# Kernel tuning notes

Hardware: AMD Instinct MI355X
Metric: run time of the kernel (lower is better)

Reference implementation:

```python
import jax, jax.numpy as jnp
import numpy as np
from jax import lax

EPS = 1e-8

def _cosine_cost(x, y):
    # 1 - cosine_similarity over feature dim: [B,N,M]
    xn = x / jnp.clip(jnp.linalg.norm(x, axis=-1, keepdims=True), EPS)
    yn = y / jnp.clip(jnp.linalg.norm(y, axis=-1, keepdims=True), EPS)
    return 1.0 - jnp.einsum('bnd,bmd->bnm', xn, yn)

def _dtw_table(cost):
    # cost: [B,N,M] -> cumulative cost tc: [B,N,M]
    # tc[i,j] = cost[i,j] + min(tc[i-1,j-1], tc[i-1,j], tc[i,j-1])
    B, N, M = cost.shape
    row0 = jnp.cumsum(cost[:, 0, :], axis=1)  # [B,M]

    def col_step(left, inp):
        c, pdiag, pup = inp  # each [B]
        v = c + jnp.minimum(jnp.minimum(pdiag, pup), left)
        return v, v

    def row_step(prev, cost_row):
        # prev, cost_row: [B,M]
        first = prev[:, 0] + cost_row[:, 0]  # [B]
        xs = (cost_row[:, 1:].T, prev[:, :-1].T, prev[:, 1:].T)  # [M-1,B]
        _, rest = lax.scan(col_step, first, xs)  # [M-1,B]
        row = jnp.concatenate([first[:, None], rest.T], axis=1)  # [B,M]
        return row, row

    _, rows = lax.scan(row_step, row0, jnp.swapaxes(cost[:, 1:, :], 0, 1))
    tc = jnp.concatenate([row0[:, None, :], jnp.swapaxes(rows, 0, 1)], axis=1)
    return tc

def _backtrack(tc):
    # tc: [N,M] -> 0/1 path matrix [N,M]; tie-break diag > up > left,
    # matching the torch equality-chain order.
    N, M = tc.shape
    path0 = jnp.zeros((N, M), tc.dtype).at[N - 1, M - 1].set(1.0)

    def cond(s):
        i, j, _ = s
        return jnp.logical_and(i > 0, j > 0)

    def body(s):
        i, j, p = s
        a = tc[i - 1, j - 1]
        b = tc[i - 1, j]
        c = tc[i, j - 1]
        diag = jnp.logical_and(a <= b, a <= c)
        up = jnp.logical_and(jnp.logical_not(diag), b <= c)
        ni = jnp.where(jnp.logical_or(diag, up), i - 1, i)
        nj = jnp.where(jnp.logical_or(diag, jnp.logical_not(up)), j - 1, j)
        p = p.at[ni, nj].set(1.0)
        return ni, nj, p

    _, _, p = lax.while_loop(cond, body, (jnp.int32(N - 1), jnp.int32(M - 1), path0))
    return p.at[0, 0].set(1.0)

def setup_inputs() -> dict:
    key = jax.random.key(0)
    kx, ky = jax.random.split(key)
    B, N, M, D = 64, 512, 512, 256
    x = jax.random.normal(kx, (B, N, D), dtype=jnp.float32)
    y = jax.random.normal(ky, (B, M, D), dtype=jnp.float32)
    return {"x": x, "y": y}

def reference(x, y):
    cost = _cosine_cost(x, y)                 # [B,N,M]
    tc = _dtw_table(cost)                     # [B,N,M]
    path = jax.vmap(_backtrack)(tc)           # [B,N,M]
    pos = jax.nn.logsumexp(jnp.sum(cost * path, axis=1), axis=1)  # [B]
    neg = jax.nn.logsumexp(jnp.sum(cost, axis=1), axis=1)         # [B]
    return pos - neg
```

## Files before the change

### kernel.cpp

```cpp
#include <hip/hip_runtime.h>
#include <hip/hip_bf16.h>
#include <stdint.h>

typedef __attribute__((ext_vector_type(8))) short short8v;
typedef __attribute__((ext_vector_type(4))) float float4v;
typedef __attribute__((ext_vector_type(4))) unsigned short ushort4v;
typedef __attribute__((ext_vector_type(4))) unsigned int uint4v;

#define FINF __builtin_huge_valf()
#define BB 64
#define NN 512
#define DD 256
#define TT_SKEW 640


static __device__ __forceinline__ unsigned short f2bf(float f) {
  union { float f; uint32_t u; } a; a.f = f;
  uint32_t r = a.u + 0x7fffu + ((a.u >> 16) & 1u);
  return (unsigned short)(r >> 16);
}
static __device__ __forceinline__ float bf2f(uint16_t v) {
  return __uint_as_float(((uint32_t)v) << 16);
}

__global__ __launch_bounds__(64) void pad_zero_kernel(uint16_t* __restrict__ skew)
{
  const int tau = blockIdx.x, b = blockIdx.y, g = threadIdx.x;
  const int r = tau - 2 * g;
  if (r < 0 || r > 511) {
    uint16_t* p = skew + ((size_t)b * TT_SKEW + tau) * NN + g * 8;
    *(uint4v*)p = (uint4v){0u, 0u, 0u, 0u};
  }
}

__global__ __launch_bounds__(256) void norm_cast_kernel(
    const float* __restrict__ x, const float* __restrict__ y,
    uint16_t* __restrict__ xnb, uint16_t* __restrict__ ynb)
{
  const int wave = threadIdx.x >> 6, lane = threadIdx.x & 63;
  const int row = blockIdx.x * 4 + wave;
  const float* src; uint16_t* dst;
  if (row < BB * NN) { src = x + (size_t)row * DD;            dst = xnb + (size_t)row * DD; }
  else               { src = y + (size_t)(row - BB*NN) * DD;  dst = ynb + (size_t)(row - BB*NN) * DD; }
  const float4v v = *(const float4v*)(src + lane * 4);
  float s = v[0]*v[0] + v[1]*v[1] + v[2]*v[2] + v[3]*v[3];
  #pragma unroll
  for (int d = 1; d < 64; d <<= 1) s += __shfl_xor(s, d, 64);
  const float inv = 1.0f / fmaxf(sqrtf(s), 1e-8f);
  ushort4v o;
  o[0] = f2bf(v[0] * inv); o[1] = f2bf(v[1] * inv);
  o[2] = f2bf(v[2] * inv); o[3] = f2bf(v[3] * inv);
  *(ushort4v*)(dst + lane * 4) = o;
}

__global__ __launch_bounds__(256) void gemm_cost_kernel(
    const uint16_t* __restrict__ xnb, const uint16_t* __restrict__ ynb,
    uint16_t* __restrict__ skew)
{
  __shared__ uint16_t As[128 * 32];
  __shared__ uint16_t Bs[128 * 32];
  const int bid = blockIdx.x;
  const int b = bid >> 4, tm = (bid >> 2) & 3, tn = bid & 3;
  const int tid = threadIdx.x, wave = tid >> 6, lane = tid & 63;
  const int wr = wave >> 1, wc = wave & 1;

  const char* Ab = (const char*)(xnb + (size_t)b * NN * DD + (size_t)tm * 128 * DD);
  const char* Bb = (const char*)(ynb + (size_t)b * NN * DD + (size_t)tn * 128 * DD);

  float4v acc[4][4];
  #pragma unroll
  for (int i = 0; i < 4; i++)
    #pragma unroll
    for (int j = 0; j < 4; j++) acc[i][j] = (float4v){0.f, 0.f, 0.f, 0.f};

  const int seg0 = wave * 2;
  const int o0 = seg0 * 1024 + lane * 16;
  const int o1 = o0 + 1024;
  const int r0 = o0 >> 6, c0 = o0 & 63;
  const int r1 = o1 >> 6, c1 = o1 & 63;

  for (int kk = 0; kk < 8; kk++) {
    const int kb = kk * 64;
    __builtin_amdgcn_global_load_lds(
        (const __attribute__((address_space(1))) uint32_t*)(Ab + (size_t)r0 * 512 + kb + c0),
        (__attribute__((address_space(3))) uint32_t*)((char*)As + seg0 * 1024), 16, 0, 0);
    __builtin_amdgcn_global_load_lds(
        (const __attribute__((address_space(1))) uint32_t*)(Ab + (size_t)r1 * 512 + kb + c1),
        (__attribute__((address_space(3))) uint32_t*)((char*)As + (seg0 + 1) * 1024), 16, 0, 0);
    __builtin_amdgcn_global_load_lds(
        (const __attribute__((address_space(1))) uint32_t*)(Bb + (size_t)r0 * 512 + kb + c0),
        (__attribute__((address_space(3))) uint32_t*)((char*)Bs + seg0 * 1024), 16, 0, 0);
    __builtin_amdgcn_global_load_lds(
        (const __attribute__((address_space(1))) uint32_t*)(Bb + (size_t)r1 * 512 + kb + c1),
        (__attribute__((address_space(3))) uint32_t*)((char*)Bs + (seg0 + 1) * 1024), 16, 0, 0);
    __syncthreads();

    short8v af[4], bfr[4];
    #pragma unroll
    for (int mi = 0; mi < 4; mi++) {
      const int rr = wr * 64 + mi * 16 + (lane & 15);
      af[mi] = *(const short8v*)((const char*)As + rr * 64 + (lane >> 4) * 16);
    }
    #pragma unroll
    for (int nj = 0; nj < 4; nj++) {
      const int rr = wc * 64 + nj * 16 + (lane & 15);
      bfr[nj] = *(const short8v*)((const char*)Bs + rr * 64 + (lane >> 4) * 16);
    }
    #pragma unroll
    for (int mi = 0; mi < 4; mi++)
      #pragma unroll
      for (int nj = 0; nj < 4; nj++)
        acc[mi][nj] = __builtin_amdgcn_mfma_f32_16x16x32_bf16(af[mi], bfr[nj], acc[mi][nj], 0, 0, 0);
    __syncthreads();
  }

  uint16_t* Cb = skew + (size_t)b * TT_SKEW * NN;
  #pragma unroll
  for (int mi = 0; mi < 4; mi++)
    #pragma unroll
    for (int nj = 0; nj < 4; nj++) {
      const int cc = tn * 128 + wc * 64 + nj * 16 + (lane & 15);
      const int lg = cc >> 3;
      #pragma unroll
      for (int v = 0; v < 4; v++) {
        const int rr = tm * 128 + wr * 64 + mi * 16 + (lane >> 4) * 4 + v;
        Cb[(size_t)(rr + 2 * lg) * NN + cc] = f2bf(1.0f - acc[mi][nj][v]);
      }
    }
}

__global__ __launch_bounds__(256) void neg_lse_kernel(
    const uint16_t* __restrict__ skew, float* __restrict__ negbuf)
{
  __shared__ float sm[8];
  const int b = blockIdx.x, tid = threadIdx.x;
  const int wave = tid >> 6, lane = tid & 63;
  const uint32_t* p = (const uint32_t*)(skew + (size_t)b * TT_SKEW * NN) + tid;
  float s0 = 0.f, s1 = 0.f;
  #pragma unroll 8
  for (int t = 0; t < TT_SKEW; ++t) {
    const uint32_t w = p[t * 256];
    s0 += __uint_as_float(w << 16);
    s1 += __uint_as_float(w & 0xFFFF0000u);
  }
  float m = fmaxf(s0, s1);
  #pragma unroll
  for (int d = 1; d < 64; d <<= 1) m = fmaxf(m, __shfl_xor(m, d, 64));
  if (lane == 0) sm[wave] = m;
  __syncthreads();
  m = fmaxf(fmaxf(sm[0], sm[1]), fmaxf(sm[2], sm[3]));
  float e = expf(s0 - m) + expf(s1 - m);
  #pragma unroll
  for (int d = 1; d < 64; d <<= 1) e += __shfl_xor(e, d, 64);
  if (lane == 0) sm[4 + wave] = e;
  __syncthreads();
  if (tid == 0) negbuf[b] = m + logf(sm[4] + sm[5] + sm[6] + sm[7]);
}

__global__ __launch_bounds__(64, 1) void dtw_fwd_kernel(
    const uint16_t* __restrict__ skew, uint32_t* __restrict__ decg)
{
  extern __shared__ char lds_raw[];
  const int l = threadIdx.x;
  const int b = blockIdx.x;
  const uint16_t* csk = skew + (size_t)b * TT_SKEW * NN;
  const uint64_t base = (uint64_t)(uintptr_t)csk;
  const bool is0 = (l == 0);
  const uint32_t voff_base = 16u * (uint32_t)l;

  uint4v ringA[8], ringB[8];
  #pragma unroll
  for (int i = 0; i < 8; ++i) {
    const uint32_t voA = voff_base + ((uint32_t)(2 * i) << 10);
    const uint32_t voB = voA + 1024u;
    asm volatile("global_load_dwordx4 %0, %1, %2" : "=v"(ringA[i]) : "v"(voA), "s"(base));
    asm volatile("global_load_dwordx4 %0, %1, %2" : "=v"(ringB[i]) : "v"(voB), "s"(base));
  }

  float tp[8];
  #pragma unroll
  for (int c = 0; c < 8; ++c) tp[c] = FINF;
  float cl0 = FINF, cl1 = FINF, carry = FINF;
  const uint32_t dump_addr = 65536u + (((uint32_t)l) << 2);

  for (int t0 = 0; t0 < 320; t0 += 8) {
    #pragma unroll
    for (int u = 0; u < 8; ++u) {
      const int t = t0 + u;
      float shA = __shfl_up(cl0, 1, 64);
      float shB = __shfl_up(cl1, 1, 64);
      if (is0) { shA = (t == 0) ? 0.0f : FINF; shB = FINF; }
      const float sh_p0 = carry;
      carry = shB;

      asm volatile("s_waitcnt vmcnt(14)" : "+v"(ringA[u]), "+v"(ringB[u]));
      const uint4v A = ringA[u];
      const uint4v Bv = ringB[u];

      const uint32_t rlane = (uint32_t)(t - l);
      const bool valid = rlane < 256u;

      float ca[8], cbv[8], S0[8], S1[8];
      #pragma unroll
      for (int k = 0; k < 4; ++k) {
        ca[2*k]   = __uint_as_float(A[k] << 16);
        ca[2*k+1] = __uint_as_float(A[k] & 0xFFFF0000u);
        cbv[2*k]   = __uint_as_float(Bv[k] << 16);
        cbv[2*k+1] = __uint_as_float(Bv[k] & 0xFFFF0000u);
      }
      S0[0] = ca[0]; S1[0] = cbv[0];
      #pragma unroll
      for (int c = 1; c < 8; ++c) { S0[c] = S0[c-1] + ca[c]; S1[c] = S1[c-1] + cbv[c]; }

      float dcp0[8], mu0[8], w0[8], PW0[8], tn0[8];
      dcp0[0] = sh_p0;
      #pragma unroll
      for (int c = 1; c < 8; ++c) dcp0[c] = tp[c-1];
      #pragma unroll
      for (int c = 0; c < 8; ++c) mu0[c] = fminf(dcp0[c], tp[c]);
      w0[0] = mu0[0];
      #pragma unroll
      for (int c = 1; c < 8; ++c) w0[c] = mu0[c] - S0[c-1];
      PW0[0] = w0[0];
      #pragma unroll
      for (int c = 1; c < 8; ++c) PW0[c] = fminf(PW0[c-1], w0[c]);
      #pragma unroll
      for (int c = 0; c < 8; ++c) tn0[c] = fminf(PW0[c], shA) + S0[c];

      float dcp1[8], mu1[8], w1[8], PW1[8], tn1[8];
      dcp1[0] = shA;
      #pragma unroll
      for (int c = 1; c < 8; ++c) dcp1[c] = tn0[c-1];
      #pragma unroll
      for (int c = 0; c < 8; ++c) mu1[c] = fminf(dcp1[c], tn0[c]);
      w1[0] = mu1[0];
      #pragma unroll
      for (int c = 1; c < 8; ++c) w1[c] = mu1[c] - S1[c-1];
      PW1[0] = w1[0];
      #pragma unroll
      for (int c = 1; c < 8; ++c) PW1[c] = fminf(PW1[c-1], w1[c]);
      #pragma unroll
      for (int c = 0; c < 8; ++c) tn1[c] = fminf(PW1[c], shB) + S1[c];

      uint32_t word = 0;
      {
        float lc0[8], lc1[8];
        lc0[0] = shA; lc1[0] = shB;
        #pragma unroll
        for (int c = 1; c < 8; ++c) { lc0[c] = tn0[c-1]; lc1[c] = tn1[c-1]; }
        #pragma unroll
        for (int c = 0; c < 8; ++c) {
          const uint32_t e0 = (tp[c] < dcp0[c]) ? 1u : 0u;
          const uint32_t d0 = (lc0[c] < mu0[c]) ? 2u : e0;
          const uint32_t e1 = (tn0[c] < dcp1[c]) ? 1u : 0u;
          const uint32_t d1 = (lc1[c] < mu1[c]) ? 2u : e1;
          word |= (d0 << (2 * c)) | (d1 << (16 + 2 * c));
        }
      }
      const uint32_t waddr = valid ? ((rlane << 8) | (((uint32_t)l) << 2)) : dump_addr;
      *(uint32_t*)(lds_raw + waddr) = word;

      #pragma unroll
      for (int c = 0; c < 8; ++c) tp[c] = valid ? tn1[c] : tp[c];
      cl0 = valid ? tn0[7] : cl0;
      cl1 = tp[7];

      {
        int rr = 2 * (t + 8); if (rr > 638) rr = 638;
        const uint32_t voA = voff_base + ((uint32_t)rr << 10);
        const uint32_t voB = voA + 1024u;
        asm volatile("global_load_dwordx4 %0, %1, %2" : "=v"(ringA[u]) : "v"(voA), "s"(base));
        asm volatile("global_load_dwordx4 %0, %1, %2" : "=v"(ringB[u]) : "v"(voB), "s"(base));
      }
    }
  }
  asm volatile("s_waitcnt vmcnt(0)" ::: "memory");

  uint32_t* dg = decg + (size_t)b * 16384;
  #pragma unroll 4
  for (int i = 0; i < 64; ++i)
    *(uint4v*)(dg + i * 256 + l * 4) = *(const uint4v*)(lds_raw + i * 1024 + l * 16);
}

__global__ __launch_bounds__(64, 1) void dtw_bt_kernel(
    const uint16_t* __restrict__ skew, const uint32_t* __restrict__ decg,
    const float* __restrict__ negbuf, float* __restrict__ out)
{
  extern __shared__ char lds_raw[];
  uint16_t* rlo    = (uint16_t*)(lds_raw + 65536);
  uint16_t* rhi    = (uint16_t*)(lds_raw + 66560);
  float*    colpos = (float*)  (lds_raw + 67584);
  const uint32_t* dec32 = (const uint32_t*)lds_raw;

  const int l = threadIdx.x;
  const int b = blockIdx.x;
  const uint16_t* csk = skew + (size_t)b * TT_SKEW * NN;
  const uint32_t* dg = decg + (size_t)b * 16384;

  #pragma unroll 4
  for (int i = 0; i < 64; ++i)
    *(uint4v*)(lds_raw + i * 1024 + l * 16) = *(const uint4v*)(dg + i * 256 + l * 4);
  for (int r = l; r < NN; r += 64) { rlo[r] = 1; rhi[r] = 0; colpos[r] = 0.0f; }
  __syncthreads();

  if (l == 0) {
    int i = NN - 1, j = NN - 1, hicur = NN - 1;
    int cidx = -1; uint32_t cw = 0;
    while (i > 0 && j > 0) {
      const int widx = (i >> 1) * 64 + (j >> 3);
      if (widx != cidx) { cw = dec32[widx]; cidx = widx; }
      const uint32_t dd = (cw >> (((i & 1) << 4) + ((j & 7) << 1))) & 3u;
      if (dd == 2u) { j--; }
      else {
        rlo[i] = (uint16_t)j; rhi[i] = (uint16_t)hicur;
        i--;
        if (dd == 0u) j--;
        hicur = j;
      }
    }
    rlo[i] = (uint16_t)j; rhi[i] = (uint16_t)hicur;
  }
  __syncthreads();
  for (int r = l; r < NN; r += 64) {
    const int lo = rlo[r], hi = rhi[r];
    for (int j = lo; j <= hi; j++) {
      const float cv = bf2f(csk[(size_t)(r + 2 * (j >> 3)) * NN + j]);
      atomicAdd(&colpos[j], cv);
    }
  }
  if (l == 0 && rlo[0] != 0) atomicAdd(&colpos[0], bf2f(csk[0]));
  __syncthreads();

  float mv[8];
  float mx2 = -FINF;
  #pragma unroll
  for (int k = 0; k < 8; k++) { mv[k] = colpos[l + 64 * k]; mx2 = fmaxf(mx2, mv[k]); }
  #pragma unroll
  for (int d = 1; d < 64; d <<= 1) mx2 = fmaxf(mx2, __shfl_xor(mx2, d, 64));
  float se2 = 0.f;
  #pragma unroll
  for (int k = 0; k < 8; k++) se2 += expf(mv[k] - mx2);
  #pragma unroll
  for (int d = 1; d < 64; d <<= 1) se2 += __shfl_xor(se2, d, 64);
  const float pos = mx2 + logf(se2);

  if (l == 0) out[b] = pos - negbuf[b];
}

extern "C" void kernel_launch(void* const* d_in, const int* in_sizes, int n_in,
                              void* d_out, int out_size, void* d_ws, size_t ws_size,
                              hipStream_t stream)
{
  (void)in_sizes; (void)n_in; (void)out_size; (void)ws_size;
  const float* x = (const float*)d_in[0];
  const float* y = (const float*)d_in[1];
  float* out = (float*)d_out;
  char* ws = (char*)d_ws;
  uint16_t* xnb  = (uint16_t*)ws;
  uint16_t* ynb  = (uint16_t*)(ws + (size_t)16777216);
  uint16_t* skew = (uint16_t*)(ws + (size_t)33554432);
  float*  negbuf = (float*)  (ws + (size_t)75497472);
  uint32_t* decg = (uint32_t*)(ws + (size_t)75501568);

  (void)hipFuncSetAttribute((const void*)dtw_fwd_kernel,
                            hipFuncAttributeMaxDynamicSharedMemorySize, 65792);
  (void)hipFuncSetAttribute((const void*)dtw_bt_kernel,
                            hipFuncAttributeMaxDynamicSharedMemorySize, 69632);

  pad_zero_kernel<<<dim3(TT_SKEW, BB), 64, 0, stream>>>(skew);
  norm_cast_kernel<<<16384, 256, 0, stream>>>(x, y, xnb, ynb);
  gemm_cost_kernel<<<1024, 256, 0, stream>>>(xnb, ynb, skew);
  neg_lse_kernel<<<64, 256, 0, stream>>>(skew, negbuf);
  dtw_fwd_kernel<<<64, 64, 65792, stream>>>(skew, decg);
  dtw_bt_kernel<<<64, 64, 69632, stream>>>(skew, decg, negbuf, out);
}
```

Baseline: 297.9 us.

## Drop pad kernel, fuse neg LSE into backtrack, pack DTW waves per block

Removes the zero-padding kernel and the separate neg-LSE kernel. The neg-LSE column sums now run inside a 256-thread backtrack kernel that also reads only the 512 valid skew rows per lane group. The forward DTW kernel now runs eight batches per 512-thread block, writing decision words straight to global memory instead of staging them in LDS, and uses a 4-deep load ring instead of 8. Backtracking reads decision words in 4x8 chunks to cut repeated LDS loads. The risks are less latency hiding in the serial DTW loop from the shallower prefetch, scattered global stores, and correctness of the skipped padding, which now depends on the loads never consuming pad cells.

```diff
diff --git a/kernel.cpp b/kernel.cpp
--- a/kernel.cpp
+++ b/kernel.cpp
@@ -21,16 +21,6 @@
 }
 static __device__ __forceinline__ float bf2f(uint16_t v) {
   return __uint_as_float(((uint32_t)v) << 16);
-}
-
-__global__ __launch_bounds__(64) void pad_zero_kernel(uint16_t* __restrict__ skew)
-{
-  const int tau = blockIdx.x, b = blockIdx.y, g = threadIdx.x;
-  const int r = tau - 2 * g;
-  if (r < 0 || r > 511) {
-    uint16_t* p = skew + ((size_t)b * TT_SKEW + tau) * NN + g * 8;
-    *(uint4v*)p = (uint4v){0u, 0u, 0u, 0u};
-  }
 }
 
 __global__ __launch_bounds__(256) void norm_cast_kernel(
@@ -129,222 +119,227 @@
     }
 }
 
-__global__ __launch_bounds__(256) void neg_lse_kernel(
-    const uint16_t* __restrict__ skew, float* __restrict__ negbuf)
-{
-  __shared__ float sm[8];
-  const int b = blockIdx.x, tid = threadIdx.x;
-  const int wave = tid >> 6, lane = tid & 63;
-  const uint32_t* p = (const uint32_t*)(skew + (size_t)b * TT_SKEW * NN) + tid;
-  float s0 = 0.f, s1 = 0.f;
-  #pragma unroll 8
-  for (int t = 0; t < TT_SKEW; ++t) {
-    const uint32_t w = p[t * 256];
-    s0 += __uint_as_float(w << 16);
-    s1 += __uint_as_float(w & 0xFFFF0000u);
-  }
-  float m = fmaxf(s0, s1);
-  #pragma unroll
-  for (int d = 1; d < 64; d <<= 1) m = fmaxf(m, __shfl_xor(m, d, 64));
-  if (lane == 0) sm[wave] = m;
-  __syncthreads();
-  m = fmaxf(fmaxf(sm[0], sm[1]), fmaxf(sm[2], sm[3]));
-  float e = expf(s0 - m) + expf(s1 - m);
-  #pragma unroll
-  for (int d = 1; d < 64; d <<= 1) e += __shfl_xor(e, d, 64);
-  if (lane == 0) sm[4 + wave] = e;
-  __syncthreads();
-  if (tid == 0) negbuf[b] = m + logf(sm[4] + sm[5] + sm[6] + sm[7]);
-}
-
-__global__ __launch_bounds__(64, 1) void dtw_fwd_kernel(
-    const uint16_t* __restrict__ skew, uint32_t* __restrict__ decg)
-{
-  extern __shared__ char lds_raw[];
-  const int l = threadIdx.x;
-  const int b = blockIdx.x;
-  const uint16_t* csk = skew + (size_t)b * TT_SKEW * NN;
-  const uint64_t base = (uint64_t)(uintptr_t)csk;
+__global__ __launch_bounds__(512, 2) void dtw_fwd_kernel(
+    const uint16_t* __restrict__ skew, uint32_t* __restrict__ decg,
+    uint32_t* __restrict__ dumpg)
+{
+  const int tid = threadIdx.x;
+  const int wv = tid >> 6, l = tid & 63;
+  const int batch = blockIdx.x * 8 + wv;
+  const uint16_t* csk = skew + (size_t)batch * TT_SKEW * NN;
+  uint32_t* const dw = decg + (size_t)batch * 16384;
+  const uintptr_t dmp_addr = (uintptr_t)(dumpg + l);
+  const uint64_t base64 = (uint64_t)(uintptr_t)csk + 16u * (uint32_t)l;
   const bool is0 = (l == 0);
-  const uint32_t voff_base = 16u * (uint32_t)l;
-
-  uint4v ringA[8], ringB[8];
-  #pragma unroll
-  for (int i = 0; i < 8; ++i) {
-    const uint32_t voA = voff_base + ((uint32_t)(2 * i) << 10);
-    const uint32_t voB = voA + 1024u;
-    asm volatile("global_load_dwordx4 %0, %1, %2" : "=v"(ringA[i]) : "v"(voA), "s"(base));
-    asm volatile("global_load_dwordx4 %0, %1, %2" : "=v"(ringB[i]) : "v"(voB), "s"(base));
+
+  uint4v rA[4], rB[4];
+  #pragma unroll
+  for (int i = 0; i < 4; ++i) {
+    const uint64_t aA = base64 + ((uint64_t)(2 * i) << 10);
+    asm volatile("global_load_dwordx4 %0, %1, off" : "=v"(rA[i]) : "v"(aA));
+    asm volatile("global_load_dwordx4 %0, %1, off" : "=v"(rB[i]) : "v"(aA + 1024u));
   }
 
   float tp[8];
   #pragma unroll
   for (int c = 0; c < 8; ++c) tp[c] = FINF;
   float cl0 = FINF, cl1 = FINF, carry = FINF;
-  const uint32_t dump_addr = 65536u + (((uint32_t)l) << 2);
-
-  for (int t0 = 0; t0 < 320; t0 += 8) {
-    #pragma unroll
-    for (int u = 0; u < 8; ++u) {
+
+  auto STEP = [&](int t, const uint4v A, const uint4v Bv) {
+    float shA = __shfl_up(cl0, 1, 64);
+    float shB = __shfl_up(cl1, 1, 64);
+    if (is0) { shA = (t == 0) ? 0.0f : FINF; shB = FINF; }
+    const float sh_p0 = carry;
+    carry = shB;
+    const float shA1 = is0 ? FINF : shA;
+
+    const uint32_t rlane = (uint32_t)(t - l);
+    const bool valid = rlane < 256u;
+
+    float ca[8], cb[8], S0[8], S1[8];
+    #pragma unroll
+    for (int k = 0; k < 4; ++k) {
+      ca[2*k]   = __uint_as_float(A[k] << 16);
+      ca[2*k+1] = __uint_as_float(A[k] & 0xFFFF0000u);
+      cb[2*k]   = __uint_as_float(Bv[k] << 16);
+      cb[2*k+1] = __uint_as_float(Bv[k] & 0xFFFF0000u);
+    }
+    S0[0] = ca[0]; S1[0] = cb[0];
+    #pragma unroll
+    for (int c = 1; c < 8; ++c) { S0[c] = S0[c-1] + ca[c]; S1[c] = S1[c-1] + cb[c]; }
+
+    float dcp0[8], mu0[8], w0[8], PW0[8], tn0[8];
+    dcp0[0] = sh_p0;
+    #pragma unroll
+    for (int c = 1; c < 8; ++c) dcp0[c] = tp[c-1];
+    #pragma unroll
+    for (int c = 0; c < 8; ++c) mu0[c] = fminf(dcp0[c], tp[c]);
+    w0[0] = mu0[0];
+    #pragma unroll
+    for (int c = 1; c < 8; ++c) w0[c] = mu0[c] - S0[c-1];
+    PW0[0] = w0[0];
+    #pragma unroll
+    for (int c = 1; c < 8; ++c) PW0[c] = fminf(PW0[c-1], w0[c]);
+    #pragma unroll
+    for (int c = 0; c < 8; ++c) tn0[c] = fminf(PW0[c], shA) + S0[c];
+
+    float dcp1[8], mu1[8], w1[8], PW1[8], tn1[8];
+    dcp1[0] = shA1;
+    #pragma unroll
+    for (int c = 1; c < 8; ++c) dcp1[c] = tn0[c-1];
+    #pragma unroll
+    for (int c = 0; c < 8; ++c) mu1[c] = fminf(dcp1[c], tn0[c]);
+    w1[0] = mu1[0];
+    #pragma unroll
+    for (int c = 1; c < 8; ++c) w1[c] = mu1[c] - S1[c-1];
+    PW1[0] = w1[0];
+    #pragma unroll
+    for (int c = 1; c < 8; ++c) PW1[c] = fminf(PW1[c-1], w1[c]);
+    #pragma unroll
+    for (int c = 0; c < 8; ++c) tn1[c] = fminf(PW1[c], shB) + S1[c];
+
+    uint32_t word = 0;
+    {
+      float lc0[8], lc1[8];
+      lc0[0] = shA; lc1[0] = shB;
+      #pragma unroll
+      for (int c = 1; c < 8; ++c) { lc0[c] = tn0[c-1]; lc1[c] = tn1[c-1]; }
+      #pragma unroll
+      for (int c = 0; c < 8; ++c) {
+        const uint32_t e0 = (tp[c] < dcp0[c]) ? 1u : 0u;
+        const uint32_t d0 = (lc0[c] < mu0[c]) ? 2u : e0;
+        const uint32_t e1 = (tn0[c] < dcp1[c]) ? 1u : 0u;
+        const uint32_t d1 = (lc1[c] < mu1[c]) ? 2u : e1;
+        word |= (d0 << (2 * c)) | (d1 << (16 + 2 * c));
+      }
+    }
+    const uintptr_t dsta = valid ? (uintptr_t)(dw + (rlane << 6) + l) : dmp_addr;
+    *(uint32_t*)dsta = word;
+
+    #pragma unroll
+    for (int c = 0; c < 8; ++c) tp[c] = valid ? tn1[c] : tp[c];
+    cl0 = valid ? tn0[7] : cl0;
+    cl1 = tp[7];
+  };
+
+  auto RELOAD = [&](int u, int t) {
+    int rr = 2 * (t + 4); if (rr > 638) rr = 638;
+    const uint64_t aA = base64 + ((uint64_t)rr << 10);
+    asm volatile("global_load_dwordx4 %0, %1, off" : "=v"(rA[u]) : "v"(aA));
+    asm volatile("global_load_dwordx4 %0, %1, off" : "=v"(rB[u]) : "v"(aA + 1024u));
+  };
+
+  asm volatile("s_waitcnt vmcnt(6)" : "+v"(rA[0]), "+v"(rB[0]) : : "memory");
+  STEP(0, rA[0], rB[0]); RELOAD(0, 0);
+  asm volatile("s_waitcnt vmcnt(7)" : "+v"(rA[1]), "+v"(rB[1]) : : "memory");
+  STEP(1, rA[1], rB[1]); RELOAD(1, 1);
+  asm volatile("s_waitcnt vmcnt(8)" : "+v"(rA[2]), "+v"(rB[2]) : : "memory");
+  STEP(2, rA[2], rB[2]); RELOAD(2, 2);
+  asm volatile("s_waitcnt vmcnt(9)" : "+v"(rA[3]), "+v"(rB[3]) : : "memory");
+  STEP(3, rA[3], rB[3]); RELOAD(3, 3);
+
+  for (int t0 = 4; t0 < 320; t0 += 4) {
+    #pragma unroll
+    for (int u = 0; u < 4; ++u) {
       const int t = t0 + u;
-      float shA = __shfl_up(cl0, 1, 64);
-      float shB = __shfl_up(cl1, 1, 64);
-      if (is0) { shA = (t == 0) ? 0.0f : FINF; shB = FINF; }
-      const float sh_p0 = carry;
-      carry = shB;
-
-      asm volatile("s_waitcnt vmcnt(14)" : "+v"(ringA[u]), "+v"(ringB[u]));
-      const uint4v A = ringA[u];
-      const uint4v Bv = ringB[u];
-
-      const uint32_t rlane = (uint32_t)(t - l);
-      const bool valid = rlane < 256u;
-
-      float ca[8], cbv[8], S0[8], S1[8];
-      #pragma unroll
-      for (int k = 0; k < 4; ++k) {
-        ca[2*k]   = __uint_as_float(A[k] << 16);
-        ca[2*k+1] = __uint_as_float(A[k] & 0xFFFF0000u);
-        cbv[2*k]   = __uint_as_float(Bv[k] << 16);
-        cbv[2*k+1] = __uint_as_float(Bv[k] & 0xFFFF0000u);
-      }
-      S0[0] = ca[0]; S1[0] = cbv[0];
-      #pragma unroll
-      for (int c = 1; c < 8; ++c) { S0[c] = S0[c-1] + ca[c]; S1[c] = S1[c-1] + cbv[c]; }
-
-      float dcp0[8], mu0[8], w0[8], PW0[8], tn0[8];
-      dcp0[0] = sh_p0;
-      #pragma unroll
-      for (int c = 1; c < 8; ++c) dcp0[c] = tp[c-1];
-      #pragma unroll
-      for (int c = 0; c < 8; ++c) mu0[c] = fminf(dcp0[c], tp[c]);
-      w0[0] = mu0[0];
-      #pragma unroll
-      for (int c = 1; c < 8; ++c) w0[c] = mu0[c] - S0[c-1];
-      PW0[0] = w0[0];
-      #pragma unroll
-      for (int c = 1; c < 8; ++c) PW0[c] = fminf(PW0[c-1], w0[c]);
-      #pragma unroll
-      for (int c = 0; c < 8; ++c) tn0[c] = fminf(PW0[c], shA) + S0[c];
-
-      float dcp1[8], mu1[8], w1[8], PW1[8], tn1[8];
-      dcp1[0] = shA;
-      #pragma unroll
-      for (int c = 1; c < 8; ++c) dcp1[c] = tn0[c-1];
-      #pragma unroll
-      for (int c = 0; c < 8; ++c) mu1[c] = fminf(dcp1[c], tn0[c]);
-      w1[0] = mu1[0];
-      #pragma unroll
-      for (int c = 1; c < 8; ++c) w1[c] = mu1[c] - S1[c-1];
-      PW1[0] = w1[0];
-      #pragma unroll
-      for (int c = 1; c < 8; ++c) PW1[c] = fminf(PW1[c-1], w1[c]);
-      #pragma unroll
-      for (int c = 0; c < 8; ++c) tn1[c] = fminf(PW1[c], shB) + S1[c];
-
-      uint32_t word = 0;
-      {
-        float lc0[8], lc1[8];
-        lc0[0] = shA; lc1[0] = shB;
-        #pragma unroll
-        for (int c = 1; c < 8; ++c) { lc0[c] = tn0[c-1]; lc1[c] = tn1[c-1]; }
-        #pragma unroll
-        for (int c = 0; c < 8; ++c) {
-          const uint32_t e0 = (tp[c] < dcp0[c]) ? 1u : 0u;
-          const uint32_t d0 = (lc0[c] < mu0[c]) ? 2u : e0;
-          const uint32_t e1 = (tn0[c] < dcp1[c]) ? 1u : 0u;
-          const uint32_t d1 = (lc1[c] < mu1[c]) ? 2u : e1;
-          word |= (d0 << (2 * c)) | (d1 << (16 + 2 * c));
-        }
-      }
-      const uint32_t waddr = valid ? ((rlane << 8) | (((uint32_t)l) << 2)) : dump_addr;
-      *(uint32_t*)(lds_raw + waddr) = word;
-
-      #pragma unroll
-      for (int c = 0; c < 8; ++c) tp[c] = valid ? tn1[c] : tp[c];
-      cl0 = valid ? tn0[7] : cl0;
-      cl1 = tp[7];
-
-      {
-        int rr = 2 * (t + 8); if (rr > 638) rr = 638;
-        const uint32_t voA = voff_base + ((uint32_t)rr << 10);
-        const uint32_t voB = voA + 1024u;
-        asm volatile("global_load_dwordx4 %0, %1, %2" : "=v"(ringA[u]) : "v"(voA), "s"(base));
-        asm volatile("global_load_dwordx4 %0, %1, %2" : "=v"(ringB[u]) : "v"(voB), "s"(base));
-      }
+      asm volatile("s_waitcnt vmcnt(9)" : "+v"(rA[u]), "+v"(rB[u]) : : "memory");
+      STEP(t, rA[u], rB[u]);
+      RELOAD(u, t);
     }
   }
   asm volatile("s_waitcnt vmcnt(0)" ::: "memory");
-
-  uint32_t* dg = decg + (size_t)b * 16384;
-  #pragma unroll 4
-  for (int i = 0; i < 64; ++i)
-    *(uint4v*)(dg + i * 256 + l * 4) = *(const uint4v*)(lds_raw + i * 1024 + l * 16);
-}
-
-__global__ __launch_bounds__(64, 1) void dtw_bt_kernel(
+}
+
+__global__ __launch_bounds__(256, 1) void dtw_bt_kernel(
     const uint16_t* __restrict__ skew, const uint32_t* __restrict__ decg,
-    const float* __restrict__ negbuf, float* __restrict__ out)
+    float* __restrict__ out)
 {
   extern __shared__ char lds_raw[];
   uint16_t* rlo    = (uint16_t*)(lds_raw + 65536);
   uint16_t* rhi    = (uint16_t*)(lds_raw + 66560);
   float*    colpos = (float*)  (lds_raw + 67584);
+  float*    sm     = (float*)  (lds_raw + 69632);
   const uint32_t* dec32 = (const uint32_t*)lds_raw;
 
-  const int l = threadIdx.x;
+  const int tid = threadIdx.x, wave = tid >> 6, lane = tid & 63;
   const int b = blockIdx.x;
   const uint16_t* csk = skew + (size_t)b * TT_SKEW * NN;
   const uint32_t* dg = decg + (size_t)b * 16384;
 
-  #pragma unroll 4
-  for (int i = 0; i < 64; ++i)
-    *(uint4v*)(lds_raw + i * 1024 + l * 16) = *(const uint4v*)(dg + i * 256 + l * 4);
-  for (int r = l; r < NN; r += 64) { rlo[r] = 1; rhi[r] = 0; colpos[r] = 0.0f; }
-  __syncthreads();
-
-  if (l == 0) {
+  #pragma unroll
+  for (int i = 0; i < 16; ++i)
+    *(uint4v*)(lds_raw + i * 4096 + tid * 16) = *(const uint4v*)(dg + i * 1024 + tid * 4);
+  for (int r = tid; r < NN; r += 256) { rlo[r] = 1; rhi[r] = 0; colpos[r] = 0.0f; }
+
+  const int g = tid >> 2;
+  const uint32_t* p = (const uint32_t*)csk + (size_t)(2 * g) * 256 + tid;
+  float s0 = 0.f, s1 = 0.f;
+  #pragma unroll 8
+  for (int t = 0; t < 512; ++t) {
+    const uint32_t w = p[(size_t)t * 256];
+    s0 += __uint_as_float(w << 16);
+    s1 += __uint_as_float(w & 0xFFFF0000u);
+  }
+  float m = fmaxf(s0, s1);
+  #pragma unroll
+  for (int d = 1; d < 64; d <<= 1) m = fmaxf(m, __shfl_xor(m, d, 64));
+  if (lane == 0) sm[wave] = m;
+  __syncthreads();
+  m = fmaxf(fmaxf(sm[0], sm[1]), fmaxf(sm[2], sm[3]));
+  float e = expf(s0 - m) + expf(s1 - m);
+  #pragma unroll
+  for (int d = 1; d < 64; d <<= 1) e += __shfl_xor(e, d, 64);
+  if (lane == 0) sm[4 + wave] = e;
+  __syncthreads();
+  const float neg = m + logf(sm[4] + sm[5] + sm[6] + sm[7]);
+  __syncthreads();
+
+  if (tid == 0) {
     int i = NN - 1, j = NN - 1, hicur = NN - 1;
-    int cidx = -1; uint32_t cw = 0;
     while (i > 0 && j > 0) {
-      const int widx = (i >> 1) * 64 + (j >> 3);
-      if (widx != cidx) { cw = dec32[widx]; cidx = widx; }
-      const uint32_t dd = (cw >> (((i & 1) << 4) + ((j & 7) << 1))) & 3u;
-      if (dd == 2u) { j--; }
-      else {
-        rlo[i] = (uint16_t)j; rhi[i] = (uint16_t)hicur;
-        i--;
-        if (dd == 0u) j--;
-        hicur = j;
+      const int a = i >> 2, g2 = j >> 3;
+      const uint32_t w0 = dec32[a * 128 + g2];
+      const uint32_t w1 = dec32[a * 128 + 64 + g2];
+      const int ilo = a << 2, jlo = g2 << 3;
+      while (i >= ilo && j >= jlo && i > 0 && j > 0) {
+        const uint32_t w = (i & 2) ? w1 : w0;
+        const uint32_t dd = (w >> (((i & 1) << 4) + ((j & 7) << 1))) & 3u;
+        if (dd == 2u) { j--; }
+        else {
+          rlo[i] = (uint16_t)j; rhi[i] = (uint16_t)hicur;
+          i--;
+          if (dd == 0u) j--;
+          hicur = j;
+        }
       }
     }
     rlo[i] = (uint16_t)j; rhi[i] = (uint16_t)hicur;
   }
   __syncthreads();
-  for (int r = l; r < NN; r += 64) {
+
+  for (int r = tid; r < NN; r += 256) {
     const int lo = rlo[r], hi = rhi[r];
     for (int j = lo; j <= hi; j++) {
       const float cv = bf2f(csk[(size_t)(r + 2 * (j >> 3)) * NN + j]);
       atomicAdd(&colpos[j], cv);
     }
   }
-  if (l == 0 && rlo[0] != 0) atomicAdd(&colpos[0], bf2f(csk[0]));
-  __syncthreads();
-
-  float mv[8];
-  float mx2 = -FINF;
-  #pragma unroll
-  for (int k = 0; k < 8; k++) { mv[k] = colpos[l + 64 * k]; mx2 = fmaxf(mx2, mv[k]); }
-  #pragma unroll
-  for (int d = 1; d < 64; d <<= 1) mx2 = fmaxf(mx2, __shfl_xor(mx2, d, 64));
-  float se2 = 0.f;
-  #pragma unroll
-  for (int k = 0; k < 8; k++) se2 += expf(mv[k] - mx2);
-  #pragma unroll
-  for (int d = 1; d < 64; d <<= 1) se2 += __shfl_xor(se2, d, 64);
-  const float pos = mx2 + logf(se2);
-
-  if (l == 0) out[b] = pos - negbuf[b];
+  if (tid == 0 && rlo[0] != 0) atomicAdd(&colpos[0], bf2f(csk[0]));
+  __syncthreads();
+
+  const float mv0 = colpos[tid], mv1 = colpos[tid + 256];
+  float mx = fmaxf(mv0, mv1);
+  #pragma unroll
+  for (int d = 1; d < 64; d <<= 1) mx = fmaxf(mx, __shfl_xor(mx, d, 64));
+  if (lane == 0) sm[wave] = mx;
+  __syncthreads();
+  mx = fmaxf(fmaxf(sm[0], sm[1]), fmaxf(sm[2], sm[3]));
+  float e2 = expf(mv0 - mx) + expf(mv1 - mx);
+  #pragma unroll
+  for (int d = 1; d < 64; d <<= 1) e2 += __shfl_xor(e2, d, 64);
+  if (lane == 0) sm[4 + wave] = e2;
+  __syncthreads();
+  if (tid == 0) out[b] = mx + logf(sm[4] + sm[5] + sm[6] + sm[7]) - neg;
 }
 
 extern "C" void kernel_launch(void* const* d_in, const int* in_sizes, int n_in,
@@ -359,18 +354,14 @@
   uint16_t* xnb  = (uint16_t*)ws;
   uint16_t* ynb  = (uint16_t*)(ws + (size_t)16777216);
   uint16_t* skew = (uint16_t*)(ws + (size_t)33554432);
-  float*  negbuf = (float*)  (ws + (size_t)75497472);
-  uint32_t* decg = (uint32_t*)(ws + (size_t)75501568);
-
-  (void)hipFuncSetAttribute((const void*)dtw_fwd_kernel,
-                            hipFuncAttributeMaxDynamicSharedMemorySize, 65792);
+  uint32_t* dumpg = (uint32_t*)(ws + (size_t)75497472);
+  uint32_t* decg  = (uint32_t*)(ws + (size_t)75501568);
+
   (void)hipFuncSetAttribute((const void*)dtw_bt_kernel,
-                            hipFuncAttributeMaxDynamicSharedMemorySize, 69632);
-
-  pad_zero_kernel<<<dim3(TT_SKEW, BB), 64, 0, stream>>>(skew);
+                            hipFuncAttributeMaxDynamicSharedMemorySize, 69760);
+
   norm_cast_kernel<<<16384, 256, 0, stream>>>(x, y, xnb, ynb);
   gemm_cost_kernel<<<1024, 256, 0, stream>>>(xnb, ynb, skew);
-  neg_lse_kernel<<<64, 256, 0, stream>>>(skew, negbuf);
-  dtw_fwd_kernel<<<64, 64, 65792, stream>>>(skew, decg);
-  dtw_bt_kernel<<<64, 64, 69632, stream>>>(skew, decg, negbuf, out);
-}
+  dtw_fwd_kernel<<<8, 512, 0, stream>>>(skew, decg, dumpg);
+  dtw_bt_kernel<<<64, 256, 69760, stream>>>(skew, decg, out);
+}
```

Measured after the change: 365.1 us. 1.23x slower.
